# Optimization experiments

Hardware: AMD Instinct MI355X
Metric: run time of the kernel (lower is better)

Reference implementation:

```python
import jax, jax.numpy as jnp
import numpy as np

N_NODES = 100000
N_EDGES = 1600000


def setup_inputs() -> dict:
    key = jax.random.key(0)
    ks = jax.random.split(key, 8)
    in_f, hid, out_c = 128, 128, 64
    return {
        "x": jax.random.normal(ks[0], (N_NODES, in_f), jnp.float32),
        "W_self1": jax.random.normal(ks[1], (in_f, hid), jnp.float32) * 0.05,
        "W_neigh1": jax.random.normal(ks[2], (in_f, hid), jnp.float32) * 0.05,
        "b1": jnp.zeros((hid,), jnp.float32),
        "W_self2": jax.random.normal(ks[3], (hid, out_c), jnp.float32) * 0.05,
        "W_neigh2": jax.random.normal(ks[4], (hid, out_c), jnp.float32) * 0.05,
        "b2": jnp.zeros((out_c,), jnp.float32),
        "src": jax.random.randint(ks[5], (N_EDGES,), 0, N_NODES, jnp.int32),
        "dst": jax.random.randint(ks[6], (N_EDGES,), 0, N_NODES, jnp.int32),
    }


def _sage_conv(h, src, dst, inv_deg, W_self, W_neigh, b):
    # mean aggregation over incoming neighbors: gather + segment-sum + normalize
    agg = jax.ops.segment_sum(h[src], dst, num_segments=N_NODES) * inv_deg  # [N, d]
    return h @ W_self + agg @ W_neigh + b


def reference(x, W_self1, W_neigh1, b1, W_self2, W_neigh2, b2, src, dst):
    # in-degree, clamped to 1 as in DGL SAGEConv
    deg = jax.ops.segment_sum(jnp.ones((N_EDGES,), x.dtype), dst, num_segments=N_NODES)
    inv_deg = (1.0 / jnp.maximum(deg, 1.0))[:, None]  # [N, 1]

    h1 = _sage_conv(x, src, dst, inv_deg, W_self1, W_neigh1, b1)      # conv1
    h1_relu = jax.nn.relu(h1)
    h2 = _sage_conv(h1_relu, src, dst, inv_deg, W_self2, W_neigh2, b2)  # conv2
    # original returns (h, middle_feat=[h1, relu(h1), h2])
    return (h2, h1, h1_relu, h2)
```

## Files before the change

### kernel.cpp

```cpp
#include <hip/hip_runtime.h>
#include <hip/hip_bf16.h>


#define NFEAT 128

typedef __bf16 bf16x8 __attribute__((ext_vector_type(8)));
typedef float  f32x4  __attribute__((ext_vector_type(4)));
typedef unsigned short ushort8v __attribute__((ext_vector_type(8)));

static __device__ inline unsigned short f2bf(float f) {
    union { float f; unsigned int u; } v; v.f = f;
    unsigned int u = v.u;
    unsigned int r = (u + 0x7FFFu + ((u >> 16) & 1u)) >> 16;
    return (unsigned short)r;
}
static __device__ inline float bf2f(unsigned short h) {
    union { unsigned int u; float f; } v; v.u = ((unsigned int)h) << 16;
    return v.f;
}

__global__ __launch_bounds__(256) void k_deg(const int* __restrict__ dst,
                                             int* __restrict__ deg,
                                             int E, int P) {
    int part = blockIdx.x & 7;
    int slice = blockIdx.x >> 3;
    int nslices = gridDim.x >> 3;
    int per = (E + nslices - 1) / nslices;
    int beg = slice * per;
    int end = beg + per; if (end > E) end = E;
    int lo = part * P;
    int hi = lo + P;
    for (int e = beg + threadIdx.x; e < end; e += 256) {
        int d = dst[e];
        if (d >= lo && d < hi) atomicAdd(&deg[d], 1);
    }
}

__global__ __launch_bounds__(256) void k_scan1(const int* __restrict__ deg,
                                               int* __restrict__ escan,
                                               int* __restrict__ bsum, int n) {
    __shared__ int ws4[4];
    int tid = threadIdx.x;
    int base = blockIdx.x * 1024 + tid * 4;
    int d[4];
    #pragma unroll
    for (int j = 0; j < 4; ++j) d[j] = (base + j < n) ? deg[base + j] : 0;
    int s = d[0] + d[1] + d[2] + d[3];
    int lane = tid & 63, wid = tid >> 6;
    int incl = s;
    #pragma unroll
    for (int off = 1; off < 64; off <<= 1) {
        int t = __shfl_up(incl, off, 64);
        if (lane >= off) incl += t;
    }
    if (lane == 63) ws4[wid] = incl;
    __syncthreads();
    int wbase = 0;
    #pragma unroll
    for (int w = 0; w < 4; ++w) if (w < wid) wbase += ws4[w];
    int run = wbase + incl - s;
    #pragma unroll
    for (int j = 0; j < 4; ++j) {
        if (base + j < n) escan[base + j] = run;
        run += d[j];
    }
    if (tid == 255) bsum[blockIdx.x] = run;
}

__global__ __launch_bounds__(1024) void k_scan2(int* __restrict__ bsum, int nb) {
    __shared__ int ws16[16];
    int tid = threadIdx.x;
    int lane = tid & 63, wid = tid >> 6;
    int v = (tid < nb) ? bsum[tid] : 0;
    int incl = v;
    #pragma unroll
    for (int off = 1; off < 64; off <<= 1) {
        int t = __shfl_up(incl, off, 64);
        if (lane >= off) incl += t;
    }
    if (lane == 63) ws16[wid] = incl;
    __syncthreads();
    int wbase = 0;
    for (int w = 0; w < 16; ++w) if (w < wid) wbase += ws16[w];
    if (tid < nb) bsum[tid] = wbase + incl - v;
}

__global__ __launch_bounds__(256) void k_scan3(const int* __restrict__ deg,
                                               const int* __restrict__ escan,
                                               const int* __restrict__ bsum,
                                               int* __restrict__ offs,
                                               int* __restrict__ cursor,
                                               float* __restrict__ invd, int n) {
    int tid = threadIdx.x;
    int base = blockIdx.x * 1024 + tid * 4;
    int bb = bsum[blockIdx.x];
    #pragma unroll
    for (int j = 0; j < 4; ++j) {
        int i = base + j;
        if (i < n) {
            int d = deg[i];
            int off = escan[i] + bb;
            offs[i] = off;
            cursor[i] = off;
            invd[i] = 1.0f / fmaxf((float)d, 1.0f);
            if (i == n - 1) offs[n] = off + d;
        }
    }
}

__global__ __launch_bounds__(256) void k_prep(const float* __restrict__ x,
                                              unsigned short* __restrict__ xb,
                                              const float* __restrict__ Ws1,
                                              const float* __restrict__ Wn1,
                                              unsigned short* __restrict__ wb1,
                                              const float* __restrict__ Ws2,
                                              const float* __restrict__ Wn2,
                                              unsigned short* __restrict__ wb2,
                                              int total4, int C) {
    int b = blockIdx.x;
    if (b < C) {
        int i = b * 256 + threadIdx.x;
        if (i >= total4) return;
        float4 v = *(const float4*)(x + (size_t)i * 4);
        ushort4 o;
        o.x = f2bf(v.x); o.y = f2bf(v.y); o.z = f2bf(v.z); o.w = f2bf(v.w);
        *(ushort4*)(xb + (size_t)i * 4) = o;
    } else if (b < C + 128) {
        int idx = (b - C) * 256 + threadIdx.x;
        int j = idx & 7, lane = (idx >> 3) & 63, ct = (idx >> 9) & 7, ks = idx >> 12;
        int k = ks * 32 + ((lane >> 4) & 3) * 8 + j;
        int n = ct * 16 + (lane & 15);
        float v = (k < 128) ? Ws1[k * 128 + n] : Wn1[(k - 128) * 128 + n];
        wb1[idx] = f2bf(v);
    } else {
        int idx = (b - C - 128) * 256 + threadIdx.x;
        int j = idx & 7, lane = (idx >> 3) & 63, ct = (idx >> 9) & 7, ks = idx >> 12;
        int k = ks * 32 + ((lane >> 4) & 3) * 8 + j;
        int n = ct * 16 + (lane & 15);
        float v = (n < 64) ? Ws2[k * 64 + n] : Wn2[k * 64 + (n - 64)];
        wb2[idx] = f2bf(v);
    }
}

__global__ __launch_bounds__(256) void k_scatter(const int* __restrict__ src,
                                                 const int* __restrict__ dst,
                                                 int* __restrict__ cursor,
                                                 int* __restrict__ ssrc,
                                                 int E, int P) {
    int part = blockIdx.x & 7;
    int slice = blockIdx.x >> 3;
    int nslices = gridDim.x >> 3;
    int per = (E + nslices - 1) / nslices;
    int beg = slice * per;
    int end = beg + per; if (end > E) end = E;
    int lo = part * P;
    int hi = lo + P;
    for (int e = beg + threadIdx.x; e < end; e += 256) {
        int d = dst[e];
        if (d >= lo && d < hi) {
            int pos = atomicAdd(&cursor[d], 1);
            ssrc[pos] = src[e];
        }
    }
}

__global__ __launch_bounds__(256) void k_mm1f(const unsigned short* __restrict__ xb,
                                              const int* __restrict__ offs,
                                              const int* __restrict__ ssrc,
                                              const float* __restrict__ invd,
                                              const unsigned short* __restrict__ wb,
                                              const float* __restrict__ bias,
                                              float* __restrict__ h1,
                                              float* __restrict__ h1r,
                                              unsigned short* __restrict__ h1rb,
                                              int M) {
    int wave = threadIdx.x >> 6, lane = threadIdx.x & 63;
    int rowbase = blockIdx.x * 64 + wave * 16;
    int node = rowbase + (lane & 15);
    if (node >= M) node = M - 1;
    int q = (lane >> 4) & 3;
    int kq = q * 8;

    float a0[8], a1[8], a2[8], a3[8];
    #pragma unroll
    for (int jj = 0; jj < 8; ++jj) { a0[jj]=0.f; a1[jj]=0.f; a2[jj]=0.f; a3[jj]=0.f; }
    int beg = offs[node], end = offs[node + 1];
    int e = beg;
    for (; e + 2 <= end; e += 2) {
        int s0 = ssrc[e], s1 = ssrc[e + 1];
        const unsigned short* r0p = xb + (size_t)s0 * NFEAT + kq;
        const unsigned short* r1p = xb + (size_t)s1 * NFEAT + kq;
        ushort8v u0 = *(const ushort8v*)(r0p);
        ushort8v u1 = *(const ushort8v*)(r0p + 32);
        ushort8v u2 = *(const ushort8v*)(r0p + 64);
        ushort8v u3 = *(const ushort8v*)(r0p + 96);
        ushort8v w0 = *(const ushort8v*)(r1p);
        ushort8v w1 = *(const ushort8v*)(r1p + 32);
        ushort8v w2 = *(const ushort8v*)(r1p + 64);
        ushort8v w3 = *(const ushort8v*)(r1p + 96);
        #pragma unroll
        for (int jj = 0; jj < 8; ++jj) {
            a0[jj] += bf2f(u0[jj]) + bf2f(w0[jj]);
            a1[jj] += bf2f(u1[jj]) + bf2f(w1[jj]);
            a2[jj] += bf2f(u2[jj]) + bf2f(w2[jj]);
            a3[jj] += bf2f(u3[jj]) + bf2f(w3[jj]);
        }
    }
    if (e < end) {
        int s0 = ssrc[e];
        const unsigned short* rp = xb + (size_t)s0 * NFEAT + kq;
        ushort8v u0 = *(const ushort8v*)(rp);
        ushort8v u1 = *(const ushort8v*)(rp + 32);
        ushort8v u2 = *(const ushort8v*)(rp + 64);
        ushort8v u3 = *(const ushort8v*)(rp + 96);
        #pragma unroll
        for (int jj = 0; jj < 8; ++jj) {
            a0[jj] += bf2f(u0[jj]);
            a1[jj] += bf2f(u1[jj]);
            a2[jj] += bf2f(u2[jj]);
            a3[jj] += bf2f(u3[jj]);
        }
    }
    float iv = invd[node];
    ushort8v g0, g1, g2, g3;
    #pragma unroll
    for (int jj = 0; jj < 8; ++jj) {
        g0[jj] = f2bf(a0[jj] * iv); g1[jj] = f2bf(a1[jj] * iv);
        g2[jj] = f2bf(a2[jj] * iv); g3[jj] = f2bf(a3[jj] * iv);
    }
    bf16x8 ag0 = *(bf16x8*)&g0;
    bf16x8 ag1 = *(bf16x8*)&g1;
    bf16x8 ag2 = *(bf16x8*)&g2;
    bf16x8 ag3 = *(bf16x8*)&g3;

    f32x4 acc[8];
    #pragma unroll
    for (int ct = 0; ct < 8; ++ct) acc[ct] = (f32x4){0.f, 0.f, 0.f, 0.f};

    #pragma unroll 1
    for (int ks = 0; ks < 4; ++ks) {
        bf16x8 a = *(const bf16x8*)(xb + (size_t)node * NFEAT + ks * 32 + kq);
        const unsigned short* wp = wb + ((size_t)ks * 512 + lane) * 8;
        #pragma unroll
        for (int ct = 0; ct < 8; ++ct) {
            bf16x8 b = *(const bf16x8*)(wp + (size_t)ct * 512);
            acc[ct] = __builtin_amdgcn_mfma_f32_16x16x32_bf16(a, b, acc[ct], 0, 0, 0);
        }
    }
    {
        const unsigned short* wl = wb + (size_t)lane * 8;
        #pragma unroll
        for (int ct = 0; ct < 8; ++ct)
            acc[ct] = __builtin_amdgcn_mfma_f32_16x16x32_bf16(
                ag0, *(const bf16x8*)(wl + (size_t)4 * 4096 + ct * 512), acc[ct], 0, 0, 0);
        #pragma unroll
        for (int ct = 0; ct < 8; ++ct)
            acc[ct] = __builtin_amdgcn_mfma_f32_16x16x32_bf16(
                ag1, *(const bf16x8*)(wl + (size_t)5 * 4096 + ct * 512), acc[ct], 0, 0, 0);
        #pragma unroll
        for (int ct = 0; ct < 8; ++ct)
            acc[ct] = __builtin_amdgcn_mfma_f32_16x16x32_bf16(
                ag2, *(const bf16x8*)(wl + (size_t)6 * 4096 + ct * 512), acc[ct], 0, 0, 0);
        #pragma unroll
        for (int ct = 0; ct < 8; ++ct)
            acc[ct] = __builtin_amdgcn_mfma_f32_16x16x32_bf16(
                ag3, *(const bf16x8*)(wl + (size_t)7 * 4096 + ct * 512), acc[ct], 0, 0, 0);
    }

    int r0 = rowbase + q * 4;
    int col0 = lane & 15;
    #pragma unroll
    for (int ct = 0; ct < 8; ++ct) {
        int col = ct * 16 + col0;
        float bv = bias[col];
        #pragma unroll
        for (int i = 0; i < 4; ++i) {
            int row = r0 + i;
            if (row < M) {
                float v = acc[ct][i] + bv;
                float vr = fmaxf(v, 0.f);
                size_t o = (size_t)row * 128 + col;
                __builtin_nontemporal_store(v, &h1[o]);
                __builtin_nontemporal_store(vr, &h1r[o]);
                h1rb[o] = f2bf(vr);
            }
        }
    }
}

__global__ __launch_bounds__(256) void k_mm2(const unsigned short* __restrict__ h1rb,
                                             const unsigned short* __restrict__ wb,
                                             float* __restrict__ s2,
                                             unsigned short* __restrict__ p2b,
                                             int M) {
    int wave = threadIdx.x >> 6, lane = threadIdx.x & 63;
    int rowbase = blockIdx.x * 64 + wave * 16;
    f32x4 acc[8];
    #pragma unroll
    for (int ct = 0; ct < 8; ++ct) acc[ct] = (f32x4){0.f, 0.f, 0.f, 0.f};

    int arow = rowbase + (lane & 15);
    if (arow >= M) arow = M - 1;
    int kq = ((lane >> 4) & 3) * 8;

    #pragma unroll 1
    for (int ks = 0; ks < 4; ++ks) {
        bf16x8 a = *(const bf16x8*)(h1rb + (size_t)arow * 128 + ks * 32 + kq);
        const unsigned short* wp = wb + ((size_t)ks * 512 + lane) * 8;
        #pragma unroll
        for (int ct = 0; ct < 8; ++ct) {
            bf16x8 b = *(const bf16x8*)(wp + (size_t)ct * 512);
            acc[ct] = __builtin_amdgcn_mfma_f32_16x16x32_bf16(a, b, acc[ct], 0, 0, 0);
        }
    }

    int r0 = rowbase + ((lane >> 4) & 3) * 4;
    int col0 = lane & 15;
    #pragma unroll
    for (int ct = 0; ct < 8; ++ct) {
        int col = ct * 16 + col0;
        #pragma unroll
        for (int i = 0; i < 4; ++i) {
            int row = r0 + i;
            if (row < M) {
                float v = acc[ct][i];
                if (col < 64)
                    s2[(size_t)row * 64 + col] = v;
                else
                    p2b[(size_t)row * 64 + (col - 64)] = f2bf(v);
            }
        }
    }
}

__global__ __launch_bounds__(256) void k_agg2(const unsigned short* __restrict__ p2b,
                                              const int* __restrict__ offs,
                                              const int* __restrict__ ssrc,
                                              const float* __restrict__ invd,
                                              const float* __restrict__ s2,
                                              const float* __restrict__ b2,
                                              float* __restrict__ h2a,
                                              float* __restrict__ h2b, int n) {
    int node = blockIdx.x * 16 + (threadIdx.x >> 4);
    if (node >= n) return;
    int lane = threadIdx.x & 15;
    int beg = offs[node], end = offs[node + 1];
    float p0 = 0.f, p1 = 0.f, p2 = 0.f, p3 = 0.f;
    float q0 = 0.f, q1 = 0.f, q2 = 0.f, q3 = 0.f;
    float r0 = 0.f, r1 = 0.f, r2 = 0.f, r3 = 0.f;
    float t0 = 0.f, t1 = 0.f, t2 = 0.f, t3 = 0.f;
    int e = beg;
    for (; e + 8 <= end; e += 8) {
        int s0 = ssrc[e + 0], s1 = ssrc[e + 1], s2i = ssrc[e + 2], s3 = ssrc[e + 3];
        int s4 = ssrc[e + 4], s5 = ssrc[e + 5], s6 = ssrc[e + 6], s7 = ssrc[e + 7];
        ushort4 v0 = *(const ushort4*)(p2b + (size_t)s0 * 64 + lane * 4);
        ushort4 v1 = *(const ushort4*)(p2b + (size_t)s1 * 64 + lane * 4);
        ushort4 v2 = *(const ushort4*)(p2b + (size_t)s2i * 64 + lane * 4);
        ushort4 v3 = *(const ushort4*)(p2b + (size_t)s3 * 64 + lane * 4);
        ushort4 v4 = *(const ushort4*)(p2b + (size_t)s4 * 64 + lane * 4);
        ushort4 v5 = *(const ushort4*)(p2b + (size_t)s5 * 64 + lane * 4);
        ushort4 v6 = *(const ushort4*)(p2b + (size_t)s6 * 64 + lane * 4);
        ushort4 v7 = *(const ushort4*)(p2b + (size_t)s7 * 64 + lane * 4);
        p0 += bf2f(v0.x); p1 += bf2f(v0.y); p2 += bf2f(v0.z); p3 += bf2f(v0.w);
        q0 += bf2f(v1.x); q1 += bf2f(v1.y); q2 += bf2f(v1.z); q3 += bf2f(v1.w);
        r0 += bf2f(v2.x); r1 += bf2f(v2.y); r2 += bf2f(v2.z); r3 += bf2f(v2.w);
        t0 += bf2f(v3.x); t1 += bf2f(v3.y); t2 += bf2f(v3.z); t3 += bf2f(v3.w);
        p0 += bf2f(v4.x); p1 += bf2f(v4.y); p2 += bf2f(v4.z); p3 += bf2f(v4.w);
        q0 += bf2f(v5.x); q1 += bf2f(v5.y); q2 += bf2f(v5.z); q3 += bf2f(v5.w);
        r0 += bf2f(v6.x); r1 += bf2f(v6.y); r2 += bf2f(v6.z); r3 += bf2f(v6.w);
        t0 += bf2f(v7.x); t1 += bf2f(v7.y); t2 += bf2f(v7.z); t3 += bf2f(v7.w);
    }
    for (; e + 4 <= end; e += 4) {
        int s0 = ssrc[e + 0], s1 = ssrc[e + 1], s2i = ssrc[e + 2], s3 = ssrc[e + 3];
        ushort4 v0 = *(const ushort4*)(p2b + (size_t)s0 * 64 + lane * 4);
        ushort4 v1 = *(const ushort4*)(p2b + (size_t)s1 * 64 + lane * 4);
        ushort4 v2 = *(const ushort4*)(p2b + (size_t)s2i * 64 + lane * 4);
        ushort4 v3 = *(const ushort4*)(p2b + (size_t)s3 * 64 + lane * 4);
        p0 += bf2f(v0.x); p1 += bf2f(v0.y); p2 += bf2f(v0.z); p3 += bf2f(v0.w);
        q0 += bf2f(v1.x); q1 += bf2f(v1.y); q2 += bf2f(v1.z); q3 += bf2f(v1.w);
        r0 += bf2f(v2.x); r1 += bf2f(v2.y); r2 += bf2f(v2.z); r3 += bf2f(v2.w);
        t0 += bf2f(v3.x); t1 += bf2f(v3.y); t2 += bf2f(v3.z); t3 += bf2f(v3.w);
    }
    for (; e < end; ++e) {
        int s = ssrc[e];
        ushort4 v = *(const ushort4*)(p2b + (size_t)s * 64 + lane * 4);
        p0 += bf2f(v.x); p1 += bf2f(v.y); p2 += bf2f(v.z); p3 += bf2f(v.w);
    }
    float a0 = (p0 + q0) + (r0 + t0);
    float a1 = (p1 + q1) + (r1 + t1);
    float a2 = (p2 + q2) + (r2 + t2);
    float a3 = (p3 + q3) + (r3 + t3);
    float iv = invd[node];
    float4 sv = *(const float4*)(s2 + (size_t)node * 64 + lane * 4);
    float4 bv = *(const float4*)(b2 + lane * 4);
    f32x4 r;
    r[0] = sv.x + a0 * iv + bv.x;
    r[1] = sv.y + a1 * iv + bv.y;
    r[2] = sv.z + a2 * iv + bv.z;
    r[3] = sv.w + a3 * iv + bv.w;
    __builtin_nontemporal_store(r, (f32x4*)(h2a + (size_t)node * 64 + lane * 4));
    __builtin_nontemporal_store(r, (f32x4*)(h2b + (size_t)node * 64 + lane * 4));
}

static inline size_t align256(size_t x) { return (x + 255) & ~(size_t)255; }

extern "C" void kernel_launch(void* const* d_in, const int* in_sizes, int n_in,
                              void* d_out, int out_size, void* d_ws, size_t ws_size,
                              hipStream_t stream) {
    const float* x   = (const float*)d_in[0];
    const float* Ws1 = (const float*)d_in[1];
    const float* Wn1 = (const float*)d_in[2];
    const float* b1  = (const float*)d_in[3];
    const float* Ws2 = (const float*)d_in[4];
    const float* Wn2 = (const float*)d_in[5];
    const float* b2  = (const float*)d_in[6];
    const int* src   = (const int*)d_in[7];
    const int* dst   = (const int*)d_in[8];

    int E = in_sizes[7];
    int N = in_sizes[0] / NFEAT;

    float* out = (float*)d_out;
    float* h2a = out;
    float* h1  = out + (size_t)N * 64;
    float* h1r = out + (size_t)N * 192;
    float* h2b = out + (size_t)N * 320;

    char* ws = (char*)d_ws;
    size_t off = 0;
    int*   deg    = (int*)(ws + off);  off = align256(off + (size_t)4 * N);
    int*   offs   = (int*)(ws + off);  off = align256(off + (size_t)4 * (N + 1));
    int*   cursor = (int*)(ws + off);  off = align256(off + (size_t)4 * N);
    float* invd   = (float*)(ws + off); off = align256(off + (size_t)4 * N);
    int*   escan  = (int*)(ws + off);  off = align256(off + (size_t)4 * N);
    int*   bsum   = (int*)(ws + off);  off = align256(off + (size_t)4 * 1024);
    int*   ssrc   = (int*)(ws + off);  off = align256(off + (size_t)4 * E);
    unsigned short* wb1 = (unsigned short*)(ws + off); off = align256(off + 2 * 32768);
    unsigned short* wb2 = (unsigned short*)(ws + off); off = align256(off + 2 * 16384);
    unsigned short* xb = (unsigned short*)(ws + off);
    float*          s2 = (float*)(ws + off);
    off = align256(off + (size_t)N * NFEAT * 2);
    unsigned short* p2b = (unsigned short*)(ws + off);
    off = align256(off + (size_t)N * 64 * 2);
    unsigned short* h1rb = (unsigned short*)(ws + off);
    off += (size_t)N * NFEAT * 2;

    int nb = (N + 1023) / 1024;
    int P = (N + 7) / 8;
    int C = (N * 32 + 255) / 256;

    hipMemsetAsync(deg, 0, (size_t)4 * N, stream);
    k_deg<<<8 * 256, 256, 0, stream>>>(dst, deg, E, P);
    k_scan1<<<nb, 256, 0, stream>>>(deg, escan, bsum, N);
    k_scan2<<<1, 1024, 0, stream>>>(bsum, nb);
    k_scan3<<<nb, 256, 0, stream>>>(deg, escan, bsum, offs, cursor, invd, N);
    k_prep<<<C + 192, 256, 0, stream>>>(x, xb, Ws1, Wn1, wb1, Ws2, Wn2, wb2,
                                        N * 32, C);
    k_scatter<<<8 * 256, 256, 0, stream>>>(src, dst, cursor, ssrc, E, P);

    k_mm1f<<<(N + 63) / 64, 256, 0, stream>>>(xb, offs, ssrc, invd, wb1, b1,
                                              h1, h1r, h1rb, N);
    k_mm2<<<(N + 63) / 64, 256, 0, stream>>>(h1rb, wb2, s2, p2b, N);
    k_agg2<<<(N + 15) / 16, 256, 0, stream>>>(p2b, offs, ssrc, invd, s2, b2, h2a, h2b, N);
}
```

Baseline: 515.9 us.

## Fuse layer-2 projection GEMM into layer-1 kernel via swizzled LDS tile

The layer-1 aggregate+GEMM kernel now writes relu(h1) as bf16 into a 16KB XOR-swizzled shared-memory tile instead of a global h1rb buffer. After a block barrier it runs the layer-2 self/neighbour projection MFMAs directly from LDS. This removes one kernel launch and the global write and re-read of the bf16 h1 activations. In exchange the fused kernel uses more LDS and registers, which may lower occupancy. s2 also gets its own workspace region instead of aliasing xb, since xb is still live when s2 is written.

```diff
diff --git a/kernel.cpp b/kernel.cpp
--- a/kernel.cpp
+++ b/kernel.cpp
@@ -164,16 +164,19 @@
     }
 }
 
-__global__ __launch_bounds__(256) void k_mm1f(const unsigned short* __restrict__ xb,
-                                              const int* __restrict__ offs,
-                                              const int* __restrict__ ssrc,
-                                              const float* __restrict__ invd,
-                                              const unsigned short* __restrict__ wb,
-                                              const float* __restrict__ bias,
-                                              float* __restrict__ h1,
-                                              float* __restrict__ h1r,
-                                              unsigned short* __restrict__ h1rb,
-                                              int M) {
+__global__ __launch_bounds__(256) void k_mmf(const unsigned short* __restrict__ xb,
+                                             const int* __restrict__ offs,
+                                             const int* __restrict__ ssrc,
+                                             const float* __restrict__ invd,
+                                             const unsigned short* __restrict__ wb,
+                                             const float* __restrict__ bias,
+                                             const unsigned short* __restrict__ wb2,
+                                             float* __restrict__ h1,
+                                             float* __restrict__ h1r,
+                                             float* __restrict__ s2,
+                                             unsigned short* __restrict__ p2b,
+                                             int M) {
+    __shared__ unsigned short lh[64 * 128];
     int wave = threadIdx.x >> 6, lane = threadIdx.x & 63;
     int rowbase = blockIdx.x * 64 + wave * 16;
     int node = rowbase + (lane & 15);
@@ -268,6 +271,7 @@
     }
 
     int r0 = rowbase + q * 4;
+    int lr0 = wave * 16 + q * 4;
     int col0 = lane & 15;
     #pragma unroll
     for (int ct = 0; ct < 8; ++ct) {
@@ -276,46 +280,34 @@
         #pragma unroll
         for (int i = 0; i < 4; ++i) {
             int row = r0 + i;
+            float v = acc[ct][i] + bv;
+            float vr = fmaxf(v, 0.f);
+            int lr = lr0 + i;
+            lh[(lr * 128 + col) ^ ((lr & 7) << 3)] = f2bf(vr);
             if (row < M) {
-                float v = acc[ct][i] + bv;
-                float vr = fmaxf(v, 0.f);
                 size_t o = (size_t)row * 128 + col;
                 __builtin_nontemporal_store(v, &h1[o]);
                 __builtin_nontemporal_store(vr, &h1r[o]);
-                h1rb[o] = f2bf(vr);
             }
         }
     }
-}
-
-__global__ __launch_bounds__(256) void k_mm2(const unsigned short* __restrict__ h1rb,
-                                             const unsigned short* __restrict__ wb,
-                                             float* __restrict__ s2,
-                                             unsigned short* __restrict__ p2b,
-                                             int M) {
-    int wave = threadIdx.x >> 6, lane = threadIdx.x & 63;
-    int rowbase = blockIdx.x * 64 + wave * 16;
-    f32x4 acc[8];
-    #pragma unroll
-    for (int ct = 0; ct < 8; ++ct) acc[ct] = (f32x4){0.f, 0.f, 0.f, 0.f};
-
-    int arow = rowbase + (lane & 15);
-    if (arow >= M) arow = M - 1;
-    int kq = ((lane >> 4) & 3) * 8;
-
+    __syncthreads();
+
+    f32x4 acc2[8];
+    #pragma unroll
+    for (int ct = 0; ct < 8; ++ct) acc2[ct] = (f32x4){0.f, 0.f, 0.f, 0.f};
+    int lr = wave * 16 + (lane & 15);
     #pragma unroll 1
     for (int ks = 0; ks < 4; ++ks) {
-        bf16x8 a = *(const bf16x8*)(h1rb + (size_t)arow * 128 + ks * 32 + kq);
-        const unsigned short* wp = wb + ((size_t)ks * 512 + lane) * 8;
+        int ui = (lr * 128 + ks * 32 + kq) ^ ((lr & 7) << 3);
+        bf16x8 a = *(const bf16x8*)&lh[ui];
+        const unsigned short* wp = wb2 + ((size_t)ks * 512 + lane) * 8;
         #pragma unroll
         for (int ct = 0; ct < 8; ++ct) {
             bf16x8 b = *(const bf16x8*)(wp + (size_t)ct * 512);
-            acc[ct] = __builtin_amdgcn_mfma_f32_16x16x32_bf16(a, b, acc[ct], 0, 0, 0);
-        }
-    }
-
-    int r0 = rowbase + ((lane >> 4) & 3) * 4;
-    int col0 = lane & 15;
+            acc2[ct] = __builtin_amdgcn_mfma_f32_16x16x32_bf16(a, b, acc2[ct], 0, 0, 0);
+        }
+    }
     #pragma unroll
     for (int ct = 0; ct < 8; ++ct) {
         int col = ct * 16 + col0;
@@ -323,7 +315,7 @@
         for (int i = 0; i < 4; ++i) {
             int row = r0 + i;
             if (row < M) {
-                float v = acc[ct][i];
+                float v = acc2[ct][i];
                 if (col < 64)
                     s2[(size_t)row * 64 + col] = v;
                 else
@@ -438,12 +430,11 @@
     unsigned short* wb1 = (unsigned short*)(ws + off); off = align256(off + 2 * 32768);
     unsigned short* wb2 = (unsigned short*)(ws + off); off = align256(off + 2 * 16384);
     unsigned short* xb = (unsigned short*)(ws + off);
-    float*          s2 = (float*)(ws + off);
     off = align256(off + (size_t)N * NFEAT * 2);
+    float* s2 = (float*)(ws + off);
+    off = align256(off + (size_t)N * 64 * 4);
     unsigned short* p2b = (unsigned short*)(ws + off);
     off = align256(off + (size_t)N * 64 * 2);
-    unsigned short* h1rb = (unsigned short*)(ws + off);
-    off += (size_t)N * NFEAT * 2;
 
     int nb = (N + 1023) / 1024;
     int P = (N + 7) / 8;
@@ -458,8 +449,7 @@
                                         N * 32, C);
     k_scatter<<<8 * 256, 256, 0, stream>>>(src, dst, cursor, ssrc, E, P);
 
-    k_mm1f<<<(N + 63) / 64, 256, 0, stream>>>(xb, offs, ssrc, invd, wb1, b1,
-                                              h1, h1r, h1rb, N);
-    k_mm2<<<(N + 63) / 64, 256, 0, stream>>>(h1rb, wb2, s2, p2b, N);
+    k_mmf<<<(N + 63) / 64, 256, 0, stream>>>(xb, offs, ssrc, invd, wb1, b1, wb2,
+                                             h1, h1r, s2, p2b, N);
     k_agg2<<<(N + 15) / 16, 256, 0, stream>>>(p2b, offs, ssrc, invd, s2, b2, h2a, h2b, N);
 }
```

Result: faster. 504.3 us (-2.2%).
